# Optimization experiments

Measured on AMD Instinct MI355X. Metric: run time of the kernel, lower is better.

The kernel has to match this reference:

```python
import jax, jax.numpy as jnp
import numpy as np
import math

B, S, D, H = 2, 2048, 1024, 16
DH = D // H

def setup_inputs() -> dict:
    key = jax.random.key(0)
    k = jax.random.split(key, 6)
    scale = 1.0 / math.sqrt(D)
    x = jax.random.normal(k[0], (B, S, D), jnp.float32)
    mask = jnp.ones((B, S), jnp.int32)
    # torch.nn.Linear weights: [out_features, in_features]
    W_q = jax.random.normal(k[1], (D, D), jnp.float32) * scale
    b_q = jnp.zeros((D,), jnp.float32)
    W_v = jax.random.normal(k[2], (D, D), jnp.float32) * scale
    W_out = jax.random.normal(k[3], (D, D), jnp.float32) * scale
    b_out = jnp.zeros((D,), jnp.float32)
    return {"x": x, "W_q": W_q, "b_q": b_q, "W_v": W_v, "W_out": W_out, "b_out": b_out, "mask": mask}

def reference(x, W_q, b_q, W_v, W_out, b_out, mask):
    inv_sqrt_dh = 1.0 / math.sqrt(DH)
    # q: [B, H, S, DH]
    q = (x @ W_q.T + b_q).reshape(B, S, H, DH).transpose(0, 2, 1, 3)
    # L2-distance attention logits: -(||q_s||^2 - 2 q_s.q_t + ||q_t||^2)/sqrt(dh)
    sq = jnp.sum(q * q, axis=-1)  # [B, H, S]
    qk = jnp.einsum('bhsd,bhtd->bhst', q, q)  # [B, H, S, S]
    logits = -(sq[..., :, None] - 2.0 * qk + sq[..., None, :]) * inv_sqrt_dh
    logits = jnp.where(mask[:, None, None, :] == 0, jnp.float32(-9e15), logits)
    w = jax.nn.softmax(logits, axis=-1)  # [B, H, S, S]
    # W_q_T[h, j, i] = W_q[i, h*DH + j] -> [H, DH, D]
    W_q_T = W_q.reshape(D, H, DH).transpose(1, 2, 0)
    # v[h, i, j] = W_v[i, h*DH + j] -> [H, D, DH]
    v = W_v.reshape(D, H, DH).transpose(1, 0, 2)
    attn = jnp.einsum('bhst,bhtd->bhsd', w, q)          # [B, H, S, DH]
    attn = jnp.einsum('bhsd,hde->bhse', attn, W_q_T)    # [B, H, S, D]
    attn = jnp.einsum('bhse,hef->bhsf', attn, v) * inv_sqrt_dh  # [B, H, S, DH]
    attn = attn.transpose(0, 2, 1, 3).reshape(B, S, D)
    return x + attn @ W_out.T + b_out
```

## Files before the change

### kernel.cpp

```cpp
#include <hip/hip_runtime.h>

#define S_LEN 2048
#define D_DIM 1024
#define NH    16
#define DHEAD 64

typedef float f32x4 __attribute__((ext_vector_type(4)));
typedef __bf16 bf16x8 __attribute__((ext_vector_type(8)));
typedef unsigned short u16;
typedef unsigned int u32;
typedef unsigned short u16x8 __attribute__((ext_vector_type(8)));
typedef unsigned short u16x4 __attribute__((ext_vector_type(4)));

__device__ __forceinline__ u16 f2bf(float f) {
    union { float f; unsigned u; } c; c.f = f;
    unsigned u = c.u + 0x7fffu + ((c.u >> 16) & 1u);
    return (u16)(u >> 16);
}

#if __has_builtin(__builtin_amdgcn_exp2f)
#define EXP2(x) __builtin_amdgcn_exp2f(x)
#else
#define EXP2(x) exp2f(x)
#endif

#define C_QK  0.36067376022224085f
#define C_SQ  0.18033688011112043f

#define MFMA16(a, b, c) __builtin_amdgcn_mfma_f32_16x16x32_bf16((a), (b), (c), 0, 0, 0)

__device__ __forceinline__ u32 pack_bf(float lo, float hi) {
    union { float f; u32 u; } a, b; a.f = lo; b.f = hi;
    return (b.u & 0xFFFF0000u) | (a.u >> 16);
}

__global__ __launch_bounds__(256) void k_cvt(
    const float* __restrict__ x, const float* __restrict__ wq,
    u16* __restrict__ xb, u16* __restrict__ wqb) {
    const int bid = blockIdx.x;
    const float* s; u16* d; size_t base;
    if (bid < 2048) { s = x;  d = xb;  base = (size_t)bid * 2048 + threadIdx.x * 8; }
    else           { s = wq; d = wqb; base = (size_t)(bid - 2048) * 2048 + threadIdx.x * 8; }
    f32x4 a = *(const f32x4*)(s + base);
    f32x4 b = *(const f32x4*)(s + base + 4);
    u16x8 o;
#pragma unroll
    for (int e = 0; e < 4; ++e) { o[e] = f2bf(a[e]); o[e + 4] = f2bf(b[e]); }
    *(u16x8*)(d + base) = o;
}

__global__ __launch_bounds__(256) void k_precomp_M(
    const float* __restrict__ Wq, const float* __restrict__ Wv, float* __restrict__ Mpart) {
    __shared__ float red[4][8][64];
    const int tid = threadIdx.x;
    const int f = tid & 63, ks = tid >> 6;
    const int jg = blockIdx.x, h = blockIdx.y, z = blockIdx.z;
    const float* vcol = Wv + h * DHEAD + f;
    const float* qcol = Wq + h * DHEAD + jg * 8;
    float acc[8];
#pragma unroll
    for (int jj = 0; jj < 8; ++jj) acc[jj] = 0.f;
    const int e0 = z * 256 + ks * 64;
    for (int e = e0; e < e0 + 64; ++e) {
        float v = vcol[(size_t)e * D_DIM];
        const float* qr = qcol + (size_t)e * D_DIM;
#pragma unroll
        for (int jj = 0; jj < 8; ++jj) acc[jj] += qr[jj] * v;
    }
#pragma unroll
    for (int jj = 0; jj < 8; ++jj) red[ks][jj][f] = acc[jj];
    __syncthreads();
    for (int t = tid; t < 512; t += 256) {
        int jj = t >> 6, ff = t & 63;
        float s = red[0][jj][ff] + red[1][jj][ff] + red[2][jj][ff] + red[3][jj][ff];
        Mpart[(size_t)z * (NH * 64 * 64) + ((size_t)(h * 64 + jg * 8 + jj)) * 64 + ff] = s * 0.125f;
    }
}

__global__ __launch_bounds__(256) void k_precomp_W2(
    const float* __restrict__ Mpart, const float* __restrict__ Wout, u16* __restrict__ W2) {
    __shared__ float Ms[64][65];
    __shared__ float Ws[64][65];
    const int tid = threadIdx.x;
    const int ob = blockIdx.x, h = blockIdx.y;
    {
        int rr = tid >> 2, seg = tid & 3;
        const size_t mo = ((size_t)(h * 64 + rr)) * 64 + seg * 16;
        const float* ws = Wout + (size_t)(ob * 64 + rr) * D_DIM + h * DHEAD + seg * 16;
#pragma unroll
        for (int e = 0; e < 16; ++e) {
            Ms[rr][seg * 16 + e] = Mpart[mo + e] + Mpart[mo + e + 65536]
                                 + Mpart[mo + e + 131072] + Mpart[mo + e + 196608];
            Ws[rr][seg * 16 + e] = ws[e];
        }
    }
    __syncthreads();
    int j = tid & 63, o0 = (tid >> 6) * 16;
    for (int oo = o0; oo < o0 + 16; ++oo) {
        float acc = 0.f;
#pragma unroll
        for (int f = 0; f < 64; ++f) acc += Ms[j][f] * Ws[oo][f];
        W2[(size_t)(ob * 64 + oo) * D_DIM + h * DHEAD + j] = f2bf(acc);
    }
}

__global__ __launch_bounds__(256) void k_qproj(
    const u16* __restrict__ xb, const u16* __restrict__ wqb,
    const float* __restrict__ bq, const int* __restrict__ mask,
    u16* __restrict__ Qbf, u16* __restrict__ QT, float* __restrict__ sq05) {
    __shared__ u16 Al[64][72];
    __shared__ u16 Bl[64][72];
    __shared__ float sqred[64];
    const int tid = threadIdx.x, lane = tid & 63, w = tid >> 6;
    const int wm = w & 1, wn = w >> 1;
    const int col16 = lane & 15, quad = lane >> 4;
    const int bm = blockIdx.x, bn = blockIdx.y;

    f32x4 acc[2][2];
    const f32x4 z4 = {0.f, 0.f, 0.f, 0.f};
#pragma unroll
    for (int i = 0; i < 2; ++i)
#pragma unroll
        for (int j = 0; j < 2; ++j) acc[i][j] = z4;

    const int ar = tid >> 2, as = tid & 3;
    const u16* pa = xb + (size_t)(bm * 64 + ar) * D_DIM + as * 16;
    const u16* pb = wqb + (size_t)(bn * 64 + ar) * D_DIM + as * 16;

    u16x8 ra[2], rb[2];
#pragma unroll
    for (int i = 0; i < 2; ++i) ra[i] = *(const u16x8*)(pa + i * 8);
#pragma unroll
    for (int i = 0; i < 2; ++i) rb[i] = *(const u16x8*)(pb + i * 8);

    for (int k0 = 0; k0 < D_DIM; k0 += 64) {
        __syncthreads();
#pragma unroll
        for (int i = 0; i < 2; ++i) *(u16x8*)&Al[ar][as * 16 + i * 8] = ra[i];
#pragma unroll
        for (int i = 0; i < 2; ++i) *(u16x8*)&Bl[ar][as * 16 + i * 8] = rb[i];
        __syncthreads();
        if (k0 + 64 < D_DIM) {
#pragma unroll
            for (int i = 0; i < 2; ++i) ra[i] = *(const u16x8*)(pa + k0 + 64 + i * 8);
#pragma unroll
            for (int i = 0; i < 2; ++i) rb[i] = *(const u16x8*)(pb + k0 + 64 + i * 8);
        }
#pragma unroll
        for (int kh = 0; kh < 2; ++kh) {
            bf16x8 af[2];
#pragma unroll
            for (int mt = 0; mt < 2; ++mt)
                af[mt] = *(const bf16x8*)&Al[wm * 32 + mt * 16 + col16][kh * 32 + quad * 8];
#pragma unroll
            for (int nt = 0; nt < 2; ++nt) {
                bf16x8 bfr = *(const bf16x8*)&Bl[wn * 32 + nt * 16 + col16][kh * 32 + quad * 8];
#pragma unroll
                for (int mt = 0; mt < 2; ++mt)
                    acc[mt][nt] = MFMA16(af[mt], bfr, acc[mt][nt]);
            }
        }
    }

    const int h = bn;
    const int bb = (bm * 64) >> 11, s0 = (bm * 64) & 2047;
    f32x4 ssum[2];
#pragma unroll
    for (int mt = 0; mt < 2; ++mt) ssum[mt] = z4;

    u16 qv16[2][2][4];
#pragma unroll
    for (int nt = 0; nt < 2; ++nt) {
        int dloc = wn * 32 + nt * 16 + col16;
        int col = bn * 64 + dloc;
        float bqv = bq[col];
#pragma unroll
        for (int mt = 0; mt < 2; ++mt) {
            int row0 = bm * 64 + wm * 32 + mt * 16 + quad * 4;
#pragma unroll
            for (int rr = 0; rr < 4; ++rr) {
                float qv = acc[mt][nt][rr] + bqv;
                ssum[mt][rr] += qv * qv;
                u16 bv = f2bf(qv);
                qv16[nt][mt][rr] = bv;
                Qbf[(size_t)(row0 + rr) * D_DIM + col] = bv;
            }
        }
    }
    float vred[2][4];
#pragma unroll
    for (int mt = 0; mt < 2; ++mt)
#pragma unroll
        for (int rr = 0; rr < 4; ++rr) {
            float v = ssum[mt][rr];
            v += __shfl_xor(v, 1); v += __shfl_xor(v, 2);
            v += __shfl_xor(v, 4); v += __shfl_xor(v, 8);
            vred[mt][rr] = v;
        }
    __syncthreads();
#pragma unroll
    for (int nt = 0; nt < 2; ++nt) {
        int dloc = wn * 32 + nt * 16 + col16;
#pragma unroll
        for (int mt = 0; mt < 2; ++mt) {
            int sl = wm * 32 + mt * 16 + quad * 4;
#pragma unroll
            for (int rr = 0; rr < 4; ++rr)
                Al[dloc][sl + rr] = qv16[nt][mt][rr];
        }
    }
    if (wn == 1 && col16 == 0) {
#pragma unroll
        for (int mt = 0; mt < 2; ++mt)
#pragma unroll
            for (int rr = 0; rr < 4; ++rr)
                sqred[wm * 32 + mt * 16 + quad * 4 + rr] = vred[mt][rr];
    }
    __syncthreads();
    if (wn == 0 && col16 == 0) {
#pragma unroll
        for (int mt = 0; mt < 2; ++mt)
#pragma unroll
            for (int rr = 0; rr < 4; ++rr) {
                int rloc = wm * 32 + mt * 16 + quad * 4 + rr;
                int sidx = s0 + rloc;
                float v = vred[mt][rr] + sqred[rloc];
                float o = mask[bb * S_LEN + sidx] ? v * C_SQ : 1e30f;
                sq05[((size_t)(bb * NH + h)) * S_LEN + sidx] = o;
            }
    }
    {
        int d = tid >> 2, ch = tid & 3;
        u16* dst = QT + ((size_t)(bb * NH + h) * DHEAD + d) * S_LEN + s0 + ch * 16;
        *(u16x8*)dst = *(const u16x8*)&Al[d][ch * 16];
        *(u16x8*)(dst + 8) = *(const u16x8*)&Al[d][ch * 16 + 8];
    }
}

__global__ __launch_bounds__(256, 2) void k_flash(
    const u16* __restrict__ Qbf, const u16* __restrict__ QT,
    const float* __restrict__ sq05, u16* __restrict__ attnO) {
    __shared__ __align__(16) char smem[34816];
    u16* Kt  = (u16*)smem;
    u16* KtT = (u16*)(smem + 16384);
    float* sql = (float*)(smem + 32768);

    const int tid = threadIdx.x, lane = tid & 63, w = tid >> 6;
    const int col16 = lane & 15, quad = lane >> 4;
    const int wq = w & 1, wk = w >> 1;
    const int qt = blockIdx.x & 15;
    const int h = (blockIdx.x >> 4) & 15;
    const int b = blockIdx.x >> 8;
    const u16* qbase = Qbf + (size_t)b * S_LEN * D_DIM + h * DHEAD;
    const u16* qtbase = QT + ((size_t)(b * NH + h)) * DHEAD * S_LEN;
    const float* sqb = sq05 + ((size_t)(b * NH + h)) * S_LEN;

    bf16x8 qb[4][2];
#pragma unroll
    for (int nq = 0; nq < 4; ++nq)
#pragma unroll
        for (int k0 = 0; k0 < 2; ++k0)
            qb[nq][k0] = *(const bf16x8*)(qbase +
                (size_t)(qt * 128 + wq * 64 + nq * 16 + col16) * D_DIM + k0 * 32 + quad * 8);

    const int r00 = wk * 64 + (col16 >> 2) * 8 + (col16 & 3);
    const int swzA = (col16 & 3) | (((col16 >> 2) & 1) << 2);
    const int krow00 = r00 * 64 + (quad ^ swzA) * 8;
    const int sq00 = wk * 64 + quad * 8;
    int vrow[4];
#pragma unroll
    for (int dblk = 0; dblk < 4; ++dblk) {
        int rT = dblk * 16 + col16;
        vrow[dblk] = rT * 128 + ((wk * 8 + quad) ^ (rT & 7)) * 8;
    }

    const int kr = tid >> 1, ks = tid & 1;
    const int td = tid >> 2, ts = tid & 3;
    const int kswz = (kr & 3) | (((kr >> 3) & 1) << 2);
    const int tswz = td & 7;
    const u16* ksrc = qbase + (size_t)kr * D_DIM + ks * 32;
    const u16* tsrc = qtbase + (size_t)td * S_LEN + ts * 32;

    u16x8 pk[4], pt[4];
    float sv = 0.f;
#pragma unroll
    for (int i = 0; i < 4; ++i) pk[i] = *(const u16x8*)(ksrc + i * 8);
#pragma unroll
    for (int i = 0; i < 4; ++i) pt[i] = *(const u16x8*)(tsrc + i * 8);
    if (tid < 128) sv = sqb[tid];

    f32x4 Oacc[4][4], lacc[4];
    const f32x4 z4 = {0.f, 0.f, 0.f, 0.f};
#pragma unroll
    for (int n = 0; n < 4; ++n) {
        lacc[n] = z4;
#pragma unroll
        for (int d = 0; d < 4; ++d) Oacc[d][n] = z4;
    }
    bf16x8 ones;
    {
        union { u16x8 u; bf16x8 b; } cv;
#pragma unroll
        for (int e = 0; e < 8; ++e) cv.u[e] = 0x3F80;
        ones = cv.b;
    }

    for (int j = 0; j < S_LEN / 128; ++j) {
        __syncthreads();
#pragma unroll
        for (int i = 0; i < 4; ++i)
            *(u16x8*)(Kt + kr * 64 + ((ks * 4 + i) ^ kswz) * 8) = pk[i];
#pragma unroll
        for (int i = 0; i < 4; ++i)
            *(u16x8*)(KtT + td * 128 + ((ts * 4 + i) ^ tswz) * 8) = pt[i];
        if (tid < 128) sql[tid] = sv;
        __syncthreads();

        int jn = (j + 1) & 15;
        {
            const u16* kn = ksrc + (size_t)jn * 128 * D_DIM;
            const u16* tn = tsrc + (size_t)jn * 128;
#pragma unroll
            for (int i = 0; i < 4; ++i) pk[i] = *(const u16x8*)(kn + i * 8);
#pragma unroll
            for (int i = 0; i < 4; ++i) pt[i] = *(const u16x8*)(tn + i * 8);
            if (tid < 128) sv = sqb[jn * 128 + tid];
        }

        for (int kt = 0; kt < 2; ++kt) {
            f32x4 sacc[2][4];
#pragma unroll
            for (int kbh = 0; kbh < 2; ++kbh)
#pragma unroll
                for (int nq = 0; nq < 4; ++nq) sacc[kbh][nq] = z4;
#pragma unroll
            for (int kbh = 0; kbh < 2; ++kbh) {
                int kro = krow00 + kt * 2048 + kbh * 256;
                bf16x8 a0 = *(const bf16x8*)(Kt + kro);
                bf16x8 a1 = *(const bf16x8*)(Kt + (kro ^ 32));
#pragma unroll
                for (int nq = 0; nq < 4; ++nq) {
                    sacc[kbh][nq] = MFMA16(a0, qb[nq][0], sacc[kbh][nq]);
                    sacc[kbh][nq] = MFMA16(a1, qb[nq][1], sacc[kbh][nq]);
                }
            }

            bf16x8 va[4];
#pragma unroll
            for (int dblk = 0; dblk < 4; ++dblk)
                va[dblk] = *(const bf16x8*)(KtT + (vrow[dblk] ^ (kt * 32)));

            u32 pf[4][4];
#pragma unroll
            for (int kbh = 0; kbh < 2; ++kbh) {
                f32x4 sqv = *(const f32x4*)(sql + sq00 + kt * 32 + kbh * 4);
#pragma unroll
                for (int nq = 0; nq < 4; ++nq) {
                    float p0 = EXP2(fmaf(sacc[kbh][nq][0], C_QK, -sqv[0]));
                    float p1 = EXP2(fmaf(sacc[kbh][nq][1], C_QK, -sqv[1]));
                    float p2 = EXP2(fmaf(sacc[kbh][nq][2], C_QK, -sqv[2]));
                    float p3 = EXP2(fmaf(sacc[kbh][nq][3], C_QK, -sqv[3]));
                    pf[nq][kbh * 2]     = pack_bf(p0, p1);
                    pf[nq][kbh * 2 + 1] = pack_bf(p2, p3);
                }
            }

#pragma unroll
            for (int nq = 0; nq < 4; ++nq) {
                union { u32 u[4]; bf16x8 b; } pb;
#pragma unroll
                for (int i = 0; i < 4; ++i) pb.u[i] = pf[nq][i];
                lacc[nq] = MFMA16(ones, pb.b, lacc[nq]);
#pragma unroll
                for (int dblk = 0; dblk < 4; ++dblk)
                    Oacc[dblk][nq] = MFMA16(va[dblk], pb.b, Oacc[dblk][nq]);
            }
        }
    }

    __syncthreads();
    float* Obuf = (float*)smem;
    float* lred = (float*)(smem + 32768);
    if (wk == 1) {
#pragma unroll
        for (int dblk = 0; dblk < 4; ++dblk)
#pragma unroll
            for (int nq = 0; nq < 4; ++nq)
                *(f32x4*)(Obuf + ((wq * 16 + dblk * 4 + nq) * 64 + lane) * 4) = Oacc[dblk][nq];
#pragma unroll
        for (int nq = 0; nq < 4; ++nq)
            lred[(wq * 4 + nq) * 64 + lane] = lacc[nq][0];
    }
    __syncthreads();
    if (wk == 0) {
        float rinv[4];
#pragma unroll
        for (int nq = 0; nq < 4; ++nq)
            rinv[nq] = 1.f / (lacc[nq][0] + lred[(wq * 4 + nq) * 64 + lane]);
        u16* obase = attnO + (size_t)b * S_LEN * D_DIM + h * DHEAD;
#pragma unroll
        for (int dblk = 0; dblk < 4; ++dblk)
#pragma unroll
            for (int nq = 0; nq < 4; ++nq) {
                f32x4 o = Oacc[dblk][nq] + *(const f32x4*)(Obuf + ((wq * 16 + dblk * 4 + nq) * 64 + lane) * 4);
                int q = qt * 128 + wq * 64 + nq * 16 + col16;
                u16x4 pkk;
#pragma unroll
                for (int rr = 0; rr < 4; ++rr) pkk[rr] = f2bf(o[rr] * rinv[nq]);
                *(u16x4*)(obase + (size_t)q * D_DIM + dblk * 16 + quad * 4) = pkk;
            }
    }
}

__global__ __launch_bounds__(256) void k_oproj(
    const u16* __restrict__ attnO, const u16* __restrict__ W2,
    const float* __restrict__ x, const float* __restrict__ bout, float* __restrict__ out) {
    __shared__ u16 Al[64][72];
    __shared__ u16 Bl[64][72];
    const int tid = threadIdx.x, lane = tid & 63, w = tid >> 6;
    const int wm = w & 1, wn = w >> 1;
    const int col16 = lane & 15, quad = lane >> 4;
    const int bm = blockIdx.x, bn = blockIdx.y;

    f32x4 acc[2][2];
    const f32x4 z4 = {0.f, 0.f, 0.f, 0.f};
#pragma unroll
    for (int i = 0; i < 2; ++i)
#pragma unroll
        for (int j = 0; j < 2; ++j) acc[i][j] = z4;

    const int ar = tid >> 2, as = tid & 3;
    const u16* pa = attnO + (size_t)(bm * 64 + ar) * D_DIM + as * 16;
    const u16* pb = W2 + (size_t)(bn * 64 + ar) * D_DIM + as * 16;

    u16x8 ra[2], rb[2];
#pragma unroll
    for (int i = 0; i < 2; ++i) ra[i] = *(const u16x8*)(pa + i * 8);
#pragma unroll
    for (int i = 0; i < 2; ++i) rb[i] = *(const u16x8*)(pb + i * 8);

    for (int k0 = 0; k0 < D_DIM; k0 += 64) {
        __syncthreads();
#pragma unroll
        for (int i = 0; i < 2; ++i) *(u16x8*)&Al[ar][as * 16 + i * 8] = ra[i];
#pragma unroll
        for (int i = 0; i < 2; ++i) *(u16x8*)&Bl[ar][as * 16 + i * 8] = rb[i];
        __syncthreads();
        if (k0 + 64 < D_DIM) {
#pragma unroll
            for (int i = 0; i < 2; ++i) ra[i] = *(const u16x8*)(pa + k0 + 64 + i * 8);
#pragma unroll
            for (int i = 0; i < 2; ++i) rb[i] = *(const u16x8*)(pb + k0 + 64 + i * 8);
        }
#pragma unroll
        for (int kh = 0; kh < 2; ++kh) {
            bf16x8 af[2];
#pragma unroll
            for (int mt = 0; mt < 2; ++mt)
                af[mt] = *(const bf16x8*)&Al[wm * 32 + mt * 16 + col16][kh * 32 + quad * 8];
#pragma unroll
            for (int nt = 0; nt < 2; ++nt) {
                bf16x8 bfr = *(const bf16x8*)&Bl[wn * 32 + nt * 16 + col16][kh * 32 + quad * 8];
#pragma unroll
                for (int mt = 0; mt < 2; ++mt)
                    acc[mt][nt] = MFMA16(af[mt], bfr, acc[mt][nt]);
            }
        }
    }
#pragma unroll
    for (int nt = 0; nt < 2; ++nt) {
        int col = bn * 64 + wn * 32 + nt * 16 + col16;
        float bv = bout[col];
#pragma unroll
        for (int mt = 0; mt < 2; ++mt) {
            int row0 = bm * 64 + wm * 32 + mt * 16 + quad * 4;
#pragma unroll
            for (int rr = 0; rr < 4; ++rr) {
                size_t idx = (size_t)(row0 + rr) * D_DIM + col;
                out[idx] = acc[mt][nt][rr] + x[idx] + bv;
            }
        }
    }
}

extern "C" void kernel_launch(void* const* d_in, const int* in_sizes, int n_in,
                              void* d_out, int out_size, void* d_ws, size_t ws_size,
                              hipStream_t stream) {
    const float* x    = (const float*)d_in[0];
    const float* Wq   = (const float*)d_in[1];
    const float* bq   = (const float*)d_in[2];
    const float* Wv   = (const float*)d_in[3];
    const float* Wout = (const float*)d_in[4];
    const float* bout = (const float*)d_in[5];
    const int*   mask = (const int*)d_in[6];
    float* out = (float*)d_out;

    char* ws = (char*)d_ws;
    u16*   Qbf   = (u16*)(ws);
    u16*   QT    = (u16*)(ws + (8u << 20));
    u16*   xb    = (u16*)(ws + (16u << 20));
    u16*   wqb   = (u16*)(ws + (24u << 20));
    u16*   W2    = (u16*)(ws + (26u << 20));
    float* Mpart = (float*)(ws + (28u << 20));
    float* sq05  = (float*)(ws + (29u << 20));
    u16*   attnO = xb;

    k_cvt<<<dim3(2560), dim3(256), 0, stream>>>(x, Wq, xb, wqb);
    k_precomp_M<<<dim3(8, 16, 4), dim3(256), 0, stream>>>(Wq, Wv, Mpart);
    k_precomp_W2<<<dim3(16, 16), dim3(256), 0, stream>>>(Mpart, Wout, W2);
    k_qproj<<<dim3(64, 16), dim3(256), 0, stream>>>(xb, wqb, bq, mask, Qbf, QT, sq05);
    k_flash<<<dim3(512), dim3(256), 0, stream>>>(Qbf, QT, sq05, attnO);
    k_oproj<<<dim3(64, 16), dim3(256), 0, stream>>>(attnO, W2, x, bout, out);
}
```

Measured before the change: 211.7 us.

## Enlarge Q and output projection GEMM tiles to 128x128 with 512 threads

The Q-projection and output-projection GEMMs move from 64x64 tiles with 256 threads to 128x128 tiles with 512 threads. Each warp now computes a 64x32 sub-tile, which raises operand reuse from shared memory and halves the number of global tile reloads. The Q-projection epilogue is rewritten to handle two heads per block: the per-row squared norms and the transposed Q output are now assembled in repurposed shared memory. The flash kernel's block index decode is reordered so consecutive blocks cover different batch/head pairs. The trade-off is fewer blocks (256 per GEMM) and higher register pressure.

```diff
diff --git a/kernel.cpp b/kernel.cpp
--- a/kernel.cpp
+++ b/kernel.cpp
@@ -104,28 +104,30 @@
     }
 }
 
-__global__ __launch_bounds__(256) void k_qproj(
+__global__ __launch_bounds__(512, 4) void k_qproj(
     const u16* __restrict__ xb, const u16* __restrict__ wqb,
     const float* __restrict__ bq, const int* __restrict__ mask,
     u16* __restrict__ Qbf, u16* __restrict__ QT, float* __restrict__ sq05) {
-    __shared__ u16 Al[64][72];
-    __shared__ u16 Bl[64][72];
-    __shared__ float sqred[64];
+    __shared__ __align__(16) char smem[38912];
+    u16* Al = (u16*)smem;
+    u16* Bl = (u16*)(smem + 18432);
+    float* sqp = (float*)(smem + 36864);
+
     const int tid = threadIdx.x, lane = tid & 63, w = tid >> 6;
     const int wm = w & 1, wn = w >> 1;
     const int col16 = lane & 15, quad = lane >> 4;
     const int bm = blockIdx.x, bn = blockIdx.y;
 
-    f32x4 acc[2][2];
+    f32x4 acc[4][2];
     const f32x4 z4 = {0.f, 0.f, 0.f, 0.f};
 #pragma unroll
-    for (int i = 0; i < 2; ++i)
+    for (int i = 0; i < 4; ++i)
 #pragma unroll
         for (int j = 0; j < 2; ++j) acc[i][j] = z4;
 
     const int ar = tid >> 2, as = tid & 3;
-    const u16* pa = xb + (size_t)(bm * 64 + ar) * D_DIM + as * 16;
-    const u16* pb = wqb + (size_t)(bn * 64 + ar) * D_DIM + as * 16;
+    const u16* pa = xb + (size_t)(bm * 128 + ar) * D_DIM + as * 16;
+    const u16* pb = wqb + (size_t)(bn * 128 + ar) * D_DIM + as * 16;
 
     u16x8 ra[2], rb[2];
 #pragma unroll
@@ -136,9 +138,9 @@
     for (int k0 = 0; k0 < D_DIM; k0 += 64) {
         __syncthreads();
 #pragma unroll
-        for (int i = 0; i < 2; ++i) *(u16x8*)&Al[ar][as * 16 + i * 8] = ra[i];
-#pragma unroll
-        for (int i = 0; i < 2; ++i) *(u16x8*)&Bl[ar][as * 16 + i * 8] = rb[i];
+        for (int i = 0; i < 2; ++i) *(u16x8*)&Al[ar * 72 + as * 16 + i * 8] = ra[i];
+#pragma unroll
+        for (int i = 0; i < 2; ++i) *(u16x8*)&Bl[ar * 72 + as * 16 + i * 8] = rb[i];
         __syncthreads();
         if (k0 + 64 < D_DIM) {
 #pragma unroll
@@ -148,35 +150,33 @@
         }
 #pragma unroll
         for (int kh = 0; kh < 2; ++kh) {
-            bf16x8 af[2];
-#pragma unroll
-            for (int mt = 0; mt < 2; ++mt)
-                af[mt] = *(const bf16x8*)&Al[wm * 32 + mt * 16 + col16][kh * 32 + quad * 8];
+            bf16x8 af[4];
+#pragma unroll
+            for (int mt = 0; mt < 4; ++mt)
+                af[mt] = *(const bf16x8*)&Al[(wm * 64 + mt * 16 + col16) * 72 + kh * 32 + quad * 8];
 #pragma unroll
             for (int nt = 0; nt < 2; ++nt) {
-                bf16x8 bfr = *(const bf16x8*)&Bl[wn * 32 + nt * 16 + col16][kh * 32 + quad * 8];
-#pragma unroll
-                for (int mt = 0; mt < 2; ++mt)
+                bf16x8 bfr = *(const bf16x8*)&Bl[(wn * 32 + nt * 16 + col16) * 72 + kh * 32 + quad * 8];
+#pragma unroll
+                for (int mt = 0; mt < 4; ++mt)
                     acc[mt][nt] = MFMA16(af[mt], bfr, acc[mt][nt]);
             }
         }
     }
 
-    const int h = bn;
-    const int bb = (bm * 64) >> 11, s0 = (bm * 64) & 2047;
-    f32x4 ssum[2];
-#pragma unroll
-    for (int mt = 0; mt < 2; ++mt) ssum[mt] = z4;
-
-    u16 qv16[2][2][4];
+    const int hh = wn >> 1;
+    f32x4 ssum[4];
+#pragma unroll
+    for (int mt = 0; mt < 4; ++mt) ssum[mt] = z4;
+
+    u16 qv16[2][4][4];
 #pragma unroll
     for (int nt = 0; nt < 2; ++nt) {
-        int dloc = wn * 32 + nt * 16 + col16;
-        int col = bn * 64 + dloc;
+        int col = bn * 128 + wn * 32 + nt * 16 + col16;
         float bqv = bq[col];
 #pragma unroll
-        for (int mt = 0; mt < 2; ++mt) {
-            int row0 = bm * 64 + wm * 32 + mt * 16 + quad * 4;
+        for (int mt = 0; mt < 4; ++mt) {
+            int row0 = bm * 128 + wm * 64 + mt * 16 + quad * 4;
 #pragma unroll
             for (int rr = 0; rr < 4; ++rr) {
                 float qv = acc[mt][nt][rr] + bqv;
@@ -187,9 +187,9 @@
             }
         }
     }
-    float vred[2][4];
-#pragma unroll
-    for (int mt = 0; mt < 2; ++mt)
+    float vred[4][4];
+#pragma unroll
+    for (int mt = 0; mt < 4; ++mt)
 #pragma unroll
         for (int rr = 0; rr < 4; ++rr) {
             float v = ssum[mt][rr];
@@ -197,43 +197,45 @@
             v += __shfl_xor(v, 4); v += __shfl_xor(v, 8);
             vred[mt][rr] = v;
         }
+    if (col16 == 0) {
+#pragma unroll
+        for (int mt = 0; mt < 4; ++mt)
+#pragma unroll
+            for (int rr = 0; rr < 4; ++rr)
+                sqp[wn * 128 + wm * 64 + mt * 16 + quad * 4 + rr] = vred[mt][rr];
+    }
     __syncthreads();
+
+    u16* Td = (u16*)smem;
 #pragma unroll
     for (int nt = 0; nt < 2; ++nt) {
-        int dloc = wn * 32 + nt * 16 + col16;
-#pragma unroll
-        for (int mt = 0; mt < 2; ++mt) {
-            int sl = wm * 32 + mt * 16 + quad * 4;
+        int dloc = (wn & 1) * 32 + nt * 16 + col16;
+#pragma unroll
+        for (int mt = 0; mt < 4; ++mt) {
+            int sl = wm * 64 + mt * 16 + quad * 4;
 #pragma unroll
             for (int rr = 0; rr < 4; ++rr)
-                Al[dloc][sl + rr] = qv16[nt][mt][rr];
-        }
-    }
-    if (wn == 1 && col16 == 0) {
-#pragma unroll
-        for (int mt = 0; mt < 2; ++mt)
-#pragma unroll
-            for (int rr = 0; rr < 4; ++rr)
-                sqred[wm * 32 + mt * 16 + quad * 4 + rr] = vred[mt][rr];
+                Td[(hh * 64 + dloc) * 130 + sl + rr] = qv16[nt][mt][rr];
+        }
     }
     __syncthreads();
-    if (wn == 0 && col16 == 0) {
-#pragma unroll
-        for (int mt = 0; mt < 2; ++mt)
-#pragma unroll
-            for (int rr = 0; rr < 4; ++rr) {
-                int rloc = wm * 32 + mt * 16 + quad * 4 + rr;
-                int sidx = s0 + rloc;
-                float v = vred[mt][rr] + sqred[rloc];
-                float o = mask[bb * S_LEN + sidx] ? v * C_SQ : 1e30f;
-                sq05[((size_t)(bb * NH + h)) * S_LEN + sidx] = o;
-            }
+
+    const int bb = (bm * 128) >> 11, s0 = (bm * 128) & 2047;
+    if (tid < 256) {
+        int r = tid & 127, hh2 = tid >> 7;
+        float v = sqp[(2 * hh2) * 128 + r] + sqp[(2 * hh2 + 1) * 128 + r];
+        int sidx = s0 + r;
+        float o = mask[bb * S_LEN + sidx] ? v * C_SQ : 1e30f;
+        sq05[((size_t)(bb * NH + bn * 2 + hh2)) * S_LEN + sidx] = o;
     }
     {
-        int d = tid >> 2, ch = tid & 3;
-        u16* dst = QT + ((size_t)(bb * NH + h) * DHEAD + d) * S_LEN + s0 + ch * 16;
-        *(u16x8*)dst = *(const u16x8*)&Al[d][ch * 16];
-        *(u16x8*)(dst + 8) = *(const u16x8*)&Al[d][ch * 16 + 8];
+        int dr = tid >> 2, ch = tid & 3;
+        int hh3 = dr >> 6, d = dr & 63;
+        u16* dst = QT + ((size_t)(bb * NH + bn * 2 + hh3) * DHEAD + d) * S_LEN + s0 + ch * 32;
+        const u16* src = Td + (hh3 * 64 + d) * 130 + ch * 32;
+#pragma unroll
+        for (int i = 0; i < 4; ++i)
+            *(u16x8*)(dst + i * 8) = *(const u16x8*)(src + i * 8);
     }
 }
 
@@ -248,9 +250,10 @@
     const int tid = threadIdx.x, lane = tid & 63, w = tid >> 6;
     const int col16 = lane & 15, quad = lane >> 4;
     const int wq = w & 1, wk = w >> 1;
-    const int qt = blockIdx.x & 15;
-    const int h = (blockIdx.x >> 4) & 15;
-    const int b = blockIdx.x >> 8;
+    const int bh = blockIdx.x & 31;
+    const int qt = blockIdx.x >> 5;
+    const int h = bh & 15;
+    const int b = bh >> 4;
     const u16* qbase = Qbf + (size_t)b * S_LEN * D_DIM + h * DHEAD;
     const u16* qtbase = QT + ((size_t)(b * NH + h)) * DHEAD * S_LEN;
     const float* sqb = sq05 + ((size_t)(b * NH + h)) * S_LEN;
@@ -412,26 +415,27 @@
     }
 }
 
-__global__ __launch_bounds__(256) void k_oproj(
+__global__ __launch_bounds__(512, 4) void k_oproj(
     const u16* __restrict__ attnO, const u16* __restrict__ W2,
     const float* __restrict__ x, const float* __restrict__ bout, float* __restrict__ out) {
-    __shared__ u16 Al[64][72];
-    __shared__ u16 Bl[64][72];
+    __shared__ __align__(16) char smem[36864];
+    u16* Al = (u16*)smem;
+    u16* Bl = (u16*)(smem + 18432);
     const int tid = threadIdx.x, lane = tid & 63, w = tid >> 6;
     const int wm = w & 1, wn = w >> 1;
     const int col16 = lane & 15, quad = lane >> 4;
     const int bm = blockIdx.x, bn = blockIdx.y;
 
-    f32x4 acc[2][2];
+    f32x4 acc[4][2];
     const f32x4 z4 = {0.f, 0.f, 0.f, 0.f};
 #pragma unroll
-    for (int i = 0; i < 2; ++i)
+    for (int i = 0; i < 4; ++i)
 #pragma unroll
         for (int j = 0; j < 2; ++j) acc[i][j] = z4;
 
     const int ar = tid >> 2, as = tid & 3;
-    const u16* pa = attnO + (size_t)(bm * 64 + ar) * D_DIM + as * 16;
-    const u16* pb = W2 + (size_t)(bn * 64 + ar) * D_DIM + as * 16;
+    const u16* pa = attnO + (size_t)(bm * 128 + ar) * D_DIM + as * 16;
+    const u16* pb = W2 + (size_t)(bn * 128 + ar) * D_DIM + as * 16;
 
     u16x8 ra[2], rb[2];
 #pragma unroll
@@ -442,9 +446,9 @@
     for (int k0 = 0; k0 < D_DIM; k0 += 64) {
         __syncthreads();
 #pragma unroll
-        for (int i = 0; i < 2; ++i) *(u16x8*)&Al[ar][as * 16 + i * 8] = ra[i];
-#pragma unroll
-        for (int i = 0; i < 2; ++i) *(u16x8*)&Bl[ar][as * 16 + i * 8] = rb[i];
+        for (int i = 0; i < 2; ++i) *(u16x8*)&Al[ar * 72 + as * 16 + i * 8] = ra[i];
+#pragma unroll
+        for (int i = 0; i < 2; ++i) *(u16x8*)&Bl[ar * 72 + as * 16 + i * 8] = rb[i];
         __syncthreads();
         if (k0 + 64 < D_DIM) {
 #pragma unroll
@@ -454,26 +458,26 @@
         }
 #pragma unroll
         for (int kh = 0; kh < 2; ++kh) {
-            bf16x8 af[2];
-#pragma unroll
-            for (int mt = 0; mt < 2; ++mt)
-                af[mt] = *(const bf16x8*)&Al[wm * 32 + mt * 16 + col16][kh * 32 + quad * 8];
+            bf16x8 af[4];
+#pragma unroll
+            for (int mt = 0; mt < 4; ++mt)
+                af[mt] = *(const bf16x8*)&Al[(wm * 64 + mt * 16 + col16) * 72 + kh * 32 + quad * 8];
 #pragma unroll
             for (int nt = 0; nt < 2; ++nt) {
-                bf16x8 bfr = *(const bf16x8*)&Bl[wn * 32 + nt * 16 + col16][kh * 32 + quad * 8];
-#pragma unroll
-                for (int mt = 0; mt < 2; ++mt)
+                bf16x8 bfr = *(const bf16x8*)&Bl[(wn * 32 + nt * 16 + col16) * 72 + kh * 32 + quad * 8];
+#pragma unroll
+                for (int mt = 0; mt < 4; ++mt)
                     acc[mt][nt] = MFMA16(af[mt], bfr, acc[mt][nt]);
             }
         }
     }
 #pragma unroll
     for (int nt = 0; nt < 2; ++nt) {
-        int col = bn * 64 + wn * 32 + nt * 16 + col16;
+        int col = bn * 128 + wn * 32 + nt * 16 + col16;
         float bv = bout[col];
 #pragma unroll
-        for (int mt = 0; mt < 2; ++mt) {
-            int row0 = bm * 64 + wm * 32 + mt * 16 + quad * 4;
+        for (int mt = 0; mt < 4; ++mt) {
+            int row0 = bm * 128 + wm * 64 + mt * 16 + quad * 4;
 #pragma unroll
             for (int rr = 0; rr < 4; ++rr) {
                 size_t idx = (size_t)(row0 + rr) * D_DIM + col;
@@ -508,7 +512,7 @@
     k_cvt<<<dim3(2560), dim3(256), 0, stream>>>(x, Wq, xb, wqb);
     k_precomp_M<<<dim3(8, 16, 4), dim3(256), 0, stream>>>(Wq, Wv, Mpart);
     k_precomp_W2<<<dim3(16, 16), dim3(256), 0, stream>>>(Mpart, Wout, W2);
-    k_qproj<<<dim3(64, 16), dim3(256), 0, stream>>>(xb, wqb, bq, mask, Qbf, QT, sq05);
+    k_qproj<<<dim3(32, 8), dim3(512), 0, stream>>>(xb, wqb, bq, mask, Qbf, QT, sq05);
     k_flash<<<dim3(512), dim3(256), 0, stream>>>(Qbf, QT, sq05, attnO);
-    k_oproj<<<dim3(64, 16), dim3(256), 0, stream>>>(attnO, W2, x, bout, out);
-}
+    k_oproj<<<dim3(32, 8), dim3(512), 0, stream>>>(attnO, W2, x, bout, out);
+}
```

Result: faster. 203.0 us (-4.1%).
